# Kernel tuning notes

Measured on AMD Instinct MI355X. Metric: run time of the kernel, lower is better.

The kernel has to match this reference:

```python
import jax, jax.numpy as jnp
import numpy as np

B, C, D = 1024, 50000, 256
LR = 0.5


def setup_inputs() -> dict:
    key = jax.random.key(0)
    kx, kl, kc = jax.random.split(key, 3)
    x = jax.random.normal(kx, (B, D), dtype=jnp.float32)
    labels = jax.random.randint(kl, (B,), 0, C)
    y = jax.nn.one_hot(labels, C, dtype=jnp.float32)  # [B, C] one-hot
    center = jax.random.normal(kc, (C, D), dtype=jnp.float32) * 0.05
    return {"x": x, "y": y, "center": center}


def reference(x, y, center):
    # dists = x - y @ center : gather each sample's class center via one-hot GEMM
    dists = x - jnp.matmul(y, center)                      # [B, D]
    # center gradient: scatter-add of -dists into class rows via one-hot GEMM
    grads = jnp.matmul(-y.T, dists)                        # [C, D]
    new_center = center - LR * grads                       # manual SGD update (assign_sub)
    loss = jnp.linalg.norm(dists, axis=1, keepdims=True)   # [B, 1]
    num_sams = jnp.sum(y, axis=0, keepdims=True) + 1.0     # [1, C]
    loss = loss / num_sams                                 # broadcasts to [B, C] as in original
    return loss, new_center
```

## Files before the change

kernel.cpp:

```cpp
#include <hip/hip_runtime.h>
#include <math.h>

#define BB 1024
#define CC 50000
#define DD 256
#define LRATE 0.5f

__global__ void k_init(const float4* __restrict__ center,
                       float4* __restrict__ out_center,
                       int4* __restrict__ counts) {
    int i = blockIdx.x * blockDim.x + threadIdx.x;
    const int n4 = CC * DD / 4;
    if (i < n4) out_center[i] = center[i];
    if (i < CC / 4)
        counts[i] = make_int4(0, 0, 0, 0);
}

#define CHUNK_ITERS 8
__global__ void k_labels_update(const unsigned int* __restrict__ y,
                                const float* __restrict__ x,
                                const float* __restrict__ center,
                                float* __restrict__ out_center,
                                int* __restrict__ counts,
                                float* __restrict__ loss_norm) {
    int b = blockIdx.x;
    const uint4* row = (const uint4*)(y + (size_t)b * CC);
    __shared__ int s_lab;
    __shared__ float s_part[4];
    if (threadIdx.x == 0) s_lab = -1;
    __syncthreads();

    const int C4 = CC / 4;
    for (int base = 0; base < C4; base += 256 * CHUNK_ITERS) {
        #pragma unroll
        for (int j = 0; j < CHUNK_ITERS; ++j) {
            int i = base + j * 256 + threadIdx.x;
            if (i < C4) {
                uint4 v = row[i];
                if (v.x | v.y | v.z | v.w) {
                    s_lab = 4 * i + (v.x ? 0 : (v.y ? 1 : (v.z ? 2 : 3)));
                }
            }
        }
        __syncthreads();
        int found = s_lab;
        __syncthreads();
        if (found >= 0) break;
    }

    int lab = s_lab;
    if (lab < 0) lab = 0;
    if (threadIdx.x == 0) atomicAdd(&counts[lab], 1);

    int d = threadIdx.x;
    float dist = x[(size_t)b * DD + d] - center[(size_t)lab * DD + d];
    atomicAdd(&out_center[(size_t)lab * DD + d], LRATE * dist);

    float sq = dist * dist;
    #pragma unroll
    for (int off = 32; off > 0; off >>= 1)
        sq += __shfl_down(sq, off, 64);
    if ((threadIdx.x & 63) == 0) s_part[threadIdx.x >> 6] = sq;
    __syncthreads();
    if (threadIdx.x == 0)
        loss_norm[b] = sqrtf(s_part[0] + s_part[1] + s_part[2] + s_part[3]);
}

#define ROWS_PER_BLK 16
__global__ void k_loss(const float* __restrict__ loss_norm,
                       const int* __restrict__ counts,
                       float* __restrict__ out_loss) {
    const int C4 = CC / 4;
    int c4 = blockIdx.x * blockDim.x + threadIdx.x;
    if (c4 >= C4) return;
    int4 cnt = ((const int4*)counts)[c4];
    float4 inv;
    inv.x = 1.0f / ((float)cnt.x + 1.0f);
    inv.y = 1.0f / ((float)cnt.y + 1.0f);
    inv.z = 1.0f / ((float)cnt.z + 1.0f);
    inv.w = 1.0f / ((float)cnt.w + 1.0f);
    int b0 = blockIdx.y * ROWS_PER_BLK;
    #pragma unroll
    for (int r = 0; r < ROWS_PER_BLK; ++r) {
        int b = b0 + r;
        float ln = loss_norm[b];
        float4 o;
        o.x = ln * inv.x; o.y = ln * inv.y; o.z = ln * inv.z; o.w = ln * inv.w;
        ((float4*)(out_loss + (size_t)b * CC))[c4] = o;
    }
}

extern "C" void kernel_launch(void* const* d_in, const int* in_sizes, int n_in,
                              void* d_out, int out_size, void* d_ws, size_t ws_size,
                              hipStream_t stream) {
    const float* x      = (const float*)d_in[0];
    const unsigned int* y = (const unsigned int*)d_in[1];
    const float* center = (const float*)d_in[2];

    float* out_loss   = (float*)d_out;
    float* out_center = (float*)d_out + (size_t)BB * CC;

    int*   counts    = (int*)d_ws;
    float* loss_norm = (float*)((char*)d_ws + 256 * 1024);

    k_init<<<CC * DD / 4 / 256, 256, 0, stream>>>(
        (const float4*)center, (float4*)out_center, (int4*)counts);

    k_labels_update<<<BB, DD, 0, stream>>>(
        y, x, center, out_center, counts, loss_norm);

    dim3 lgrid((CC / 4 + 255) / 256, BB / ROWS_PER_BLK);
    k_loss<<<lgrid, 256, 0, stream>>>(loss_norm, counts, out_loss);
}
```

Measured before the change: 421.0 us.

## Split label search into a grid-wide one-hot scan kernel plus update kernel

The per-row label search, in which one block walked its one-hot row with early exit and block-wide syncs, becomes a separate flat kernel that streams the whole one-hot matrix with one uint4 per thread and writes each row's label to workspace. A second kernel then performs the center atomic update, the count update and the norm from the stored labels. This trades the early-exit saving, which read about half of y on average, for a full read of y with much higher memory-level parallelism and no serial chunk loop. It also adds one kernel launch and a small labels buffer in the workspace.

```diff
diff --git a/kernel.cpp b/kernel.cpp
--- a/kernel.cpp
+++ b/kernel.cpp
@@ -5,6 +5,9 @@
 #define CC 50000
 #define DD 256
 #define LRATE 0.5f
+
+#define C4 (CC / 4)
+#define Q4 (BB * C4)
 
 __global__ void k_init(const float4* __restrict__ center,
                        float4* __restrict__ out_center,
@@ -16,53 +19,41 @@
         counts[i] = make_int4(0, 0, 0, 0);
 }
 
-#define CHUNK_ITERS 8
-__global__ void k_labels_update(const unsigned int* __restrict__ y,
-                                const float* __restrict__ x,
-                                const float* __restrict__ center,
-                                float* __restrict__ out_center,
-                                int* __restrict__ counts,
-                                float* __restrict__ loss_norm) {
+__global__ void k_scan(const uint4* __restrict__ y4,
+                       int* __restrict__ labels) {
+    unsigned q = blockIdx.x * blockDim.x + threadIdx.x;
+    uint4 v = y4[q];
+    if (v.x | v.y | v.z | v.w) {
+        unsigned b = q / (unsigned)C4;
+        unsigned j = q - b * (unsigned)C4;
+        labels[b] = 4 * j + (v.x ? 0 : (v.y ? 1 : (v.z ? 2 : 3)));
+    }
+}
+
+__global__ void k_update(const int* __restrict__ labels,
+                         const float* __restrict__ x,
+                         const float* __restrict__ center,
+                         float* __restrict__ out_center,
+                         int* __restrict__ counts,
+                         float* __restrict__ loss_norm) {
     int b = blockIdx.x;
-    const uint4* row = (const uint4*)(y + (size_t)b * CC);
-    __shared__ int s_lab;
-    __shared__ float s_part[4];
-    if (threadIdx.x == 0) s_lab = -1;
-    __syncthreads();
-
-    const int C4 = CC / 4;
-    for (int base = 0; base < C4; base += 256 * CHUNK_ITERS) {
-        #pragma unroll
-        for (int j = 0; j < CHUNK_ITERS; ++j) {
-            int i = base + j * 256 + threadIdx.x;
-            if (i < C4) {
-                uint4 v = row[i];
-                if (v.x | v.y | v.z | v.w) {
-                    s_lab = 4 * i + (v.x ? 0 : (v.y ? 1 : (v.z ? 2 : 3)));
-                }
-            }
-        }
-        __syncthreads();
-        int found = s_lab;
-        __syncthreads();
-        if (found >= 0) break;
-    }
-
-    int lab = s_lab;
-    if (lab < 0) lab = 0;
-    if (threadIdx.x == 0) atomicAdd(&counts[lab], 1);
+    int lab = labels[b];
+    lab = (unsigned)lab >= (unsigned)CC ? 0 : lab;
 
     int d = threadIdx.x;
     float dist = x[(size_t)b * DD + d] - center[(size_t)lab * DD + d];
     atomicAdd(&out_center[(size_t)lab * DD + d], LRATE * dist);
+    if (d == 0) atomicAdd(&counts[lab], 1);
 
     float sq = dist * dist;
     #pragma unroll
     for (int off = 32; off > 0; off >>= 1)
         sq += __shfl_down(sq, off, 64);
-    if ((threadIdx.x & 63) == 0) s_part[threadIdx.x >> 6] = sq;
+
+    __shared__ float s_part[4];
+    if ((d & 63) == 0) s_part[d >> 6] = sq;
     __syncthreads();
-    if (threadIdx.x == 0)
+    if (d == 0)
         loss_norm[b] = sqrtf(s_part[0] + s_part[1] + s_part[2] + s_part[3]);
 }
 
@@ -70,9 +61,9 @@
 __global__ void k_loss(const float* __restrict__ loss_norm,
                        const int* __restrict__ counts,
                        float* __restrict__ out_loss) {
-    const int C4 = CC / 4;
+    const int c4n = CC / 4;
     int c4 = blockIdx.x * blockDim.x + threadIdx.x;
-    if (c4 >= C4) return;
+    if (c4 >= c4n) return;
     int4 cnt = ((const int4*)counts)[c4];
     float4 inv;
     inv.x = 1.0f / ((float)cnt.x + 1.0f);
@@ -93,21 +84,25 @@
 extern "C" void kernel_launch(void* const* d_in, const int* in_sizes, int n_in,
                               void* d_out, int out_size, void* d_ws, size_t ws_size,
                               hipStream_t stream) {
-    const float* x      = (const float*)d_in[0];
+    const float* x        = (const float*)d_in[0];
     const unsigned int* y = (const unsigned int*)d_in[1];
-    const float* center = (const float*)d_in[2];
+    const float* center   = (const float*)d_in[2];
 
     float* out_loss   = (float*)d_out;
     float* out_center = (float*)d_out + (size_t)BB * CC;
 
     int*   counts    = (int*)d_ws;
     float* loss_norm = (float*)((char*)d_ws + 256 * 1024);
+    int*   labels    = (int*)((char*)d_ws + 200704);
 
     k_init<<<CC * DD / 4 / 256, 256, 0, stream>>>(
         (const float4*)center, (float4*)out_center, (int4*)counts);
 
-    k_labels_update<<<BB, DD, 0, stream>>>(
-        y, x, center, out_center, counts, loss_norm);
+    k_scan<<<Q4 / 256, 256, 0, stream>>>(
+        (const uint4*)y, labels);
+
+    k_update<<<BB, DD, 0, stream>>>(
+        labels, x, center, out_center, counts, loss_norm);
 
     dim3 lgrid((CC / 4 + 255) / 256, BB / ROWS_PER_BLK);
     k_loss<<<lgrid, 256, 0, stream>>>(loss_norm, counts, out_loss);
```

After: 423.1 us. About the same (+0.5%).
